# Performance work log

Measured on AMD Instinct MI355X. Metric: run time of the kernel, lower is better.

Reference implementation:

```python
import jax, jax.numpy as jnp
import numpy as np
import math

B, N, C = 2, 1024, 81            # images, proposals per image, classes (incl. background)
IMG_W, IMG_H = 1333, 800         # image size for all images (box.size)
SCORE_THRESH = 0.05
NMS_THRESH = 0.5
DETS_PER_IMG = 100
WX, WY, WW, WH = 10.0, 10.0, 5.0, 5.0   # BoxCoder weights
BBOX_XFORM_CLIP = math.log(1000.0 / 16.0)
NEG_INF = -1e30


def setup_inputs() -> dict:
    key = jax.random.key(0)
    k1, k2, k3, k4 = jax.random.split(key, 4)
    class_logits = jax.random.normal(k1, (B * N, C), dtype=jnp.float32)
    box_regression = jax.random.normal(k2, (B * N, C * 4), dtype=jnp.float32)
    # valid xyxy proposal boxes inside the image
    xy = jax.random.uniform(k3, (B * N, 2), dtype=jnp.float32) * jnp.array([IMG_W - 150.0, IMG_H - 150.0], jnp.float32)
    wh = 10.0 + jax.random.uniform(k4, (B * N, 2), dtype=jnp.float32) * 140.0
    proposal_boxes = jnp.concatenate([xy, xy + wh], axis=-1)
    return {"class_logits": class_logits, "box_regression": box_regression, "proposal_boxes": proposal_boxes}


def box_decode(rel_codes, boxes):
    """BoxCoder.decode (maskrcnn-benchmark). rel_codes [M, 4C], boxes [M,4] xyxy -> [M, C, 4]."""
    TO_REMOVE = 1.0
    widths = boxes[:, 2] - boxes[:, 0] + TO_REMOVE
    heights = boxes[:, 3] - boxes[:, 1] + TO_REMOVE
    ctr_x = boxes[:, 0] + 0.5 * widths
    ctr_y = boxes[:, 1] + 0.5 * heights
    dx = rel_codes[:, 0::4] / WX
    dy = rel_codes[:, 1::4] / WY
    dw = jnp.minimum(rel_codes[:, 2::4] / WW, BBOX_XFORM_CLIP)
    dh = jnp.minimum(rel_codes[:, 3::4] / WH, BBOX_XFORM_CLIP)
    pred_ctr_x = dx * widths[:, None] + ctr_x[:, None]
    pred_ctr_y = dy * heights[:, None] + ctr_y[:, None]
    pred_w = jnp.exp(dw) * widths[:, None]
    pred_h = jnp.exp(dh) * heights[:, None]
    x1 = pred_ctr_x - 0.5 * pred_w
    y1 = pred_ctr_y - 0.5 * pred_h
    x2 = pred_ctr_x + 0.5 * pred_w - 1.0
    y2 = pred_ctr_y + 0.5 * pred_h - 1.0
    return jnp.stack([x1, y1, x2, y2], axis=-1)  # [M, C, 4]


def iou_matrix(b):
    """Pairwise IoU with TO_REMOVE=1 convention. b [N,4] -> [N,N]."""
    area = (b[:, 2] - b[:, 0] + 1.0) * (b[:, 3] - b[:, 1] + 1.0)
    lt = jnp.maximum(b[:, None, :2], b[None, :, :2])
    rb = jnp.minimum(b[:, None, 2:], b[None, :, 2:])
    wh = jnp.clip(rb - lt + 1.0, 0.0)
    inter = wh[..., 0] * wh[..., 1]
    return inter / (area[:, None] + area[None, :] - inter)


def nms_keep(boxes, scores, valid):
    """Masked greedy NMS: returns keep mask [N]. Invalid entries never kept/suppress."""
    s = jnp.where(valid, scores, NEG_INF)
    order = jnp.argsort(-s)            # descending score
    b = boxes[order]
    iou = iou_matrix(b)                # [N, N]
    idx = jnp.arange(N)

    def body(i, keep):
        sup = keep[i] & (iou[i] > NMS_THRESH) & (idx > i)
        return keep & ~sup

    keep_sorted = jax.lax.fori_loop(0, N, body, valid[order])
    return jnp.zeros((N,), bool).at[order].set(keep_sorted)


def per_image(prob, boxes):
    """prob [N,C], boxes [N,C,4] -> top-DETS_PER_IMG (boxes, scores, labels)."""
    fg_prob = prob[:, 1:]              # skip background (cls_start_idx=1)
    fg_boxes = boxes[:, 1:]            # [N, C-1, 4]
    valid = fg_prob > SCORE_THRESH
    # per-class masked NMS, vmapped over the class axis
    keep = jax.vmap(nms_keep, in_axes=(1, 1, 1), out_axes=1)(fg_boxes, fg_prob, valid)  # [N, C-1]
    flat_scores = jnp.where(keep, fg_prob, NEG_INF).reshape(-1)       # [(C-1)*N]
    flat_boxes = fg_boxes.reshape(-1, 4)
    flat_labels = jnp.tile(jnp.arange(1, C, dtype=jnp.int64), (N,))   # matches [N, C-1] flatten
    top_s, top_i = jax.lax.top_k(flat_scores, DETS_PER_IMG)
    valid_top = top_s > SCORE_THRESH
    out_scores = jnp.where(valid_top, top_s, 0.0)
    out_boxes = jnp.where(valid_top[:, None], flat_boxes[top_i], 0.0)
    out_labels = jnp.where(valid_top, flat_labels[top_i], -1)
    return out_boxes, out_scores, out_labels


def reference(class_logits, box_regression, proposal_boxes):
    prob = jax.nn.softmax(class_logits, axis=-1)                # [B*N, C]
    decoded = box_decode(box_regression, proposal_boxes)        # [B*N, C, 4]
    # clip_to_image (remove_empty=False), TO_REMOVE=1
    x = jnp.clip(decoded[..., 0::2], 0.0, IMG_W - 1.0)
    y = jnp.clip(decoded[..., 1::2], 0.0, IMG_H - 1.0)
    decoded = jnp.stack([x[..., 0], y[..., 0], x[..., 1], y[..., 1]], axis=-1)
    prob = prob.reshape(B, N, C)
    decoded = decoded.reshape(B, N, C, 4)
    # process images sequentially to bound the [C-1, N, N] IoU working set
    boxes_out, scores_out, labels_out = jax.lax.map(lambda a: per_image(*a), (prob, decoded))
    return boxes_out, scores_out, labels_out
```

## Files before the change

kernel.cpp:

```cpp
#include <hip/hip_runtime.h>
#include <math.h>

#define B_ 2
#define N_ 1024
#define C_ 81
#define NFG 80
#define DETS 100
#define CAND (N_ * NFG)
#define SCORE_THRESH 0.05f
#define NMS_THRESH 0.5f
#define NEG_INF -1e30f
#define IMG_W_M1 1332.0f
#define IMG_H_M1 799.0f
#define XFORM_CLIP 4.135166556742356f
#define HB 192
#define LCAP 512
#define NROW (B_ * N_)


__device__ __forceinline__ void decode_box(const float* __restrict__ breg,
                                           const float* __restrict__ pbox,
                                           int row, int c, float* out) {
    float bx1 = pbox[row * 4 + 0];
    float by1 = pbox[row * 4 + 1];
    float bx2 = pbox[row * 4 + 2];
    float by2 = pbox[row * 4 + 3];
    float w  = bx2 - bx1 + 1.0f;
    float h  = by2 - by1 + 1.0f;
    float cx = bx1 + 0.5f * w;
    float cy = by1 + 0.5f * h;
    const float* r = breg + (size_t)row * (C_ * 4) + c * 4;
    float dx = r[0] / 10.0f;
    float dy = r[1] / 10.0f;
    float dw = fminf(r[2] / 5.0f, (float)XFORM_CLIP);
    float dh = fminf(r[3] / 5.0f, (float)XFORM_CLIP);
    float px = dx * w + cx;
    float py = dy * h + cy;
    float pw = expf(dw) * w;
    float ph = expf(dh) * h;
    float x1 = px - 0.5f * pw;
    float y1 = py - 0.5f * ph;
    float x2 = px + 0.5f * pw - 1.0f;
    float y2 = py + 0.5f * ph - 1.0f;
    out[0] = fminf(fmaxf(x1, 0.0f), IMG_W_M1);
    out[1] = fminf(fmaxf(y1, 0.0f), IMG_H_M1);
    out[2] = fminf(fmaxf(x2, 0.0f), IMG_W_M1);
    out[3] = fminf(fmaxf(y2, 0.0f), IMG_H_M1);
}


__global__ __launch_bounds__(256) void prob_k(const float* __restrict__ logits,
                                              float* __restrict__ probT,
                                              int* __restrict__ count) {
    if (blockIdx.x == 0 && threadIdx.x < B_) count[threadIdx.x] = 0;
    int row  = blockIdx.x * 4 + (threadIdx.x >> 6);
    int lane = threadIdx.x & 63;
    const float* rp = logits + (size_t)row * C_;
    float v0 = rp[lane];
    float v1 = (lane + 64 < C_) ? rp[lane + 64] : -INFINITY;
    float m = fmaxf(v0, v1);
    #pragma unroll
    for (int off = 32; off; off >>= 1) m = fmaxf(m, __shfl_xor(m, off));
    float e0 = expf(v0 - m);
    float e1 = (lane + 64 < C_) ? expf(v1 - m) : 0.0f;
    float s = e0 + e1;
    #pragma unroll
    for (int off = 32; off; off >>= 1) s += __shfl_xor(s, off);
    probT[(size_t)lane * NROW + row] = e0 / s;
    if (lane + 64 < C_) probT[(size_t)(lane + 64) * NROW + row] = e1 / s;
}


__global__ __launch_bounds__(256) void nms_k(const float* __restrict__ probT,
                                             const float* __restrict__ breg,
                                             const float* __restrict__ pbox,
                                             float* __restrict__ cand_s,
                                             int* __restrict__ cand_i,
                                             int* __restrict__ count) {
    __shared__ float skey[N_];
    __shared__ int   sidx[N_];
    __shared__ float sx1[N_], sy1[N_], sx2[N_], sy2[N_], sar[N_];
    __shared__ unsigned rembits[64];
    __shared__ int   mcount;

    int blk = blockIdx.x;
    int b   = blk / NFG;
    int c   = blk % NFG + 1;
    int tid = threadIdx.x;

    if (tid == 0) mcount = 0;
    __syncthreads();

    const float* col = probT + (size_t)c * NROW + b * N_;
    #pragma unroll
    for (int r = 0; r < N_ / 256; ++r) {
        int n = tid + r * 256;
        float s = col[n];
        if (s > SCORE_THRESH) {
            int p = atomicAdd(&mcount, 1);
            skey[p] = s;
            sidx[p] = n;
        }
    }
    __syncthreads();
    int M = mcount;

    if (M > 0 && M <= 64) {
        if (tid < 64) {
            int lane = tid;
            unsigned long long key;
            if (lane < M)
                key = ((unsigned long long)(~__float_as_uint(skey[lane])) << 32) |
                      (unsigned)sidx[lane];
            else
                key = ~0ULL;
            #pragma unroll
            for (int k = 2; k <= 64; k <<= 1) {
                #pragma unroll
                for (int j = k >> 1; j > 0; j >>= 1) {
                    unsigned long long other = __shfl_xor(key, j);
                    bool lower    = (lane & j) == 0;
                    bool dir_asc  = (lane & k) == 0;
                    bool keep_min = (dir_asc == lower);
                    bool mine_min = key < other;
                    key = (keep_min == mine_min) ? key : other;
                }
            }
            float sc = __uint_as_float(~(unsigned)(key >> 32));
            int   n  = (int)(unsigned)(key & 0xFFFFFFFFu);
            float bx[4]; float area = 0.0f; int rem = 0;
            if (lane < M) {
                decode_box(breg, pbox, b * N_ + n, c, bx);
                area = (bx[2] - bx[0] + 1.0f) * (bx[3] - bx[1] + 1.0f);
            }
            for (int i = 0; i < M; ++i) {
                int   rem_i = __shfl(rem, i);
                float x1i = __shfl(bx[0], i);
                float y1i = __shfl(bx[1], i);
                float x2i = __shfl(bx[2], i);
                float y2i = __shfl(bx[3], i);
                float ai  = __shfl(area, i);
                if (!rem_i && lane > i && lane < M && !rem) {
                    float xx1 = fmaxf(x1i, bx[0]);
                    float yy1 = fmaxf(y1i, bx[1]);
                    float xx2 = fminf(x2i, bx[2]);
                    float yy2 = fminf(y2i, bx[3]);
                    float w = fmaxf(xx2 - xx1 + 1.0f, 0.0f);
                    float h = fmaxf(yy2 - yy1 + 1.0f, 0.0f);
                    float inter = w * h;
                    float iou = inter / (area + ai - inter);
                    if (iou > NMS_THRESH) rem = 1;
                }
            }
            unsigned long long keepmask = __ballot(lane < M && !rem);
            int base = 0;
            if (lane == 0) base = atomicAdd(&count[b], __popcll(keepmask));
            base = __shfl(base, 0);
            if (lane < M && !rem) {
                int pos = base + __popcll(keepmask & ((1ULL << lane) - 1ULL));
                cand_s[(size_t)b * CAND + pos] = sc;
                cand_i[(size_t)b * CAND + pos] = n * NFG + (c - 1);
            }
        }
    } else if (M > 64) {
        int P = 64;
        while (P < M) P <<= 1;
        for (int i = M + tid; i < P; i += 256) { skey[i] = NEG_INF; sidx[i] = 0x7fffffff; }
        __syncthreads();
        for (int k = 2; k <= P; k <<= 1) {
            for (int j = k >> 1; j > 0; j >>= 1) {
                for (int i = tid; i < P; i += 256) {
                    int l = i ^ j;
                    if (l > i) {
                        float ki = skey[i], kl = skey[l];
                        int   ii = sidx[i], il = sidx[l];
                        bool iFirst = (ki > kl) || (ki == kl && ii < il);
                        bool asc = ((i & k) == 0);
                        if (iFirst != asc) {
                            skey[i] = kl; skey[l] = ki;
                            sidx[i] = il; sidx[l] = ii;
                        }
                    }
                }
                __syncthreads();
            }
        }
        for (int i = tid; i < M; i += 256) {
            float box[4];
            decode_box(breg, pbox, b * N_ + sidx[i], c, box);
            sx1[i] = box[0]; sy1[i] = box[1]; sx2[i] = box[2]; sy2[i] = box[3];
            sar[i] = (box[2] - box[0] + 1.0f) * (box[3] - box[1] + 1.0f);
        }
        __syncthreads();
        if (tid < 64) {
            int lane = tid;
            unsigned my = 0;
            for (int i = 0; i < M; ++i) {
                unsigned obits = __shfl(my, i & 63);
                bool kept = ((obits >> (i >> 6)) & 1u) == 0u;
                if (kept) {
                    float x1i = sx1[i], y1i = sy1[i], x2i = sx2[i], y2i = sy2[i], ai = sar[i];
                    for (int j = lane; j < M; j += 64) {
                        if (j > i && !((my >> (j >> 6)) & 1u)) {
                            float xx1 = fmaxf(x1i, sx1[j]);
                            float yy1 = fmaxf(y1i, sy1[j]);
                            float xx2 = fminf(x2i, sx2[j]);
                            float yy2 = fminf(y2i, sy2[j]);
                            float w = fmaxf(xx2 - xx1 + 1.0f, 0.0f);
                            float h = fmaxf(yy2 - yy1 + 1.0f, 0.0f);
                            float inter = w * h;
                            float iou = inter / (ai + sar[j] - inter);
                            if (iou > NMS_THRESH) my |= 1u << (j >> 6);
                        }
                    }
                }
            }
            rembits[lane] = my;
        }
        __syncthreads();
        for (int j = tid; j < M; j += 256) {
            if (!((rembits[j & 63] >> (j >> 6)) & 1u)) {
                int pos = atomicAdd(&count[b], 1);
                cand_s[(size_t)b * CAND + pos] = skey[j];
                cand_i[(size_t)b * CAND + pos] = sidx[j] * NFG + (c - 1);
            }
        }
    }
}


#define TTPB 512

__global__ __launch_bounds__(TTPB) void topk_k(float* __restrict__ cand_s,
                                               const int* __restrict__ cand_i,
                                               const int* __restrict__ count,
                                               const float* __restrict__ breg,
                                               const float* __restrict__ pbox,
                                               float* __restrict__ out) {
    __shared__ int   hist[HB];
    __shared__ int   ssum[HB];
    __shared__ float lsv[LCAP];
    __shared__ int   lfv[LCAP];
    __shared__ int   lcnt;
    __shared__ int   sel_t1;
    __shared__ float rs[TTPB];
    __shared__ int   rf[TTPB];
    __shared__ int   rp[TTPB];

    int b   = blockIdx.x;
    int tid = threadIdx.x;
    int M2  = count[b];
    float* cs = cand_s + (size_t)b * CAND;
    const int* ci = cand_i + (size_t)b * CAND;
    float* boxes_o  = out + (size_t)b * DETS * 4;
    float* scores_o = out + (size_t)B_ * DETS * 4 + (size_t)b * DETS;
    float* labels_o = out + (size_t)B_ * DETS * 4 + (size_t)B_ * DETS + (size_t)b * DETS;

    for (int i = tid; i < HB; i += TTPB) hist[i] = 0;
    if (tid == 0) { lcnt = 0; sel_t1 = 0; }
    __syncthreads();

    for (int i = tid; i < M2; i += TTPB) {
        unsigned bits = __float_as_uint(cs[i]);
        int cb = (int)((bits - 0x3D000000u) >> 18);
        if (cb > HB - 1) cb = HB - 1;
        atomicAdd(&hist[cb], 1);
    }
    __syncthreads();

    if (tid < HB) {
        int acc = 0;
        for (int j = tid; j < HB; ++j) acc += hist[j];
        ssum[tid] = acc;
    }
    __syncthreads();
    if (M2 > DETS && tid < HB) {
        if (ssum[tid] >= DETS && (tid == HB - 1 || ssum[tid + 1] < DETS)) sel_t1 = tid;
    }
    __syncthreads();
    int t1 = sel_t1;

    for (int i = tid; i < M2; i += TTPB) {
        float s = cs[i];
        unsigned bits = __float_as_uint(s);
        int cb = (int)((bits - 0x3D000000u) >> 18);
        if (cb > HB - 1) cb = HB - 1;
        if (cb >= t1) {
            int p = atomicAdd(&lcnt, 1);
            if (p < LCAP) { lsv[p] = s; lfv[p] = ci[i]; }
        }
    }
    __syncthreads();
    int L = lcnt;

    if (L <= LCAP) {
        for (int e = tid; e < L; e += TTPB) {
            float s = lsv[e]; int f = lfv[e];
            int r = 0;
            for (int q = 0; q < L; ++q) {
                float sq = lsv[q]; int fq = lfv[q];
                if (sq > s || (sq == s && fq < f)) r++;
            }
            if (r < DETS) {
                int n = f / NFG;
                int cc = f % NFG + 1;
                float box[4];
                decode_box(breg, pbox, b * N_ + n, cc, box);
                boxes_o[r * 4 + 0] = box[0];
                boxes_o[r * 4 + 1] = box[1];
                boxes_o[r * 4 + 2] = box[2];
                boxes_o[r * 4 + 3] = box[3];
                scores_o[r] = s;
                labels_o[r] = (float)cc;
            }
        }
        int start = (L < DETS) ? L : DETS;
        for (int r = tid; r < DETS; r += TTPB) {
            if (r >= start) {
                boxes_o[r * 4 + 0] = 0.0f;
                boxes_o[r * 4 + 1] = 0.0f;
                boxes_o[r * 4 + 2] = 0.0f;
                boxes_o[r * 4 + 3] = 0.0f;
                scores_o[r] = 0.0f;
                labels_o[r] = -1.0f;
            }
        }
    } else {
        for (int it = 0; it < DETS; ++it) {
            float bs = NEG_INF; int bf = 0x7fffffff; int bp = -1;
            for (int i = tid; i < M2; i += TTPB) {
                float s = cs[i]; int f = ci[i];
                if (s > bs || (s == bs && f < bf)) { bs = s; bf = f; bp = i; }
            }
            rs[tid] = bs; rf[tid] = bf; rp[tid] = bp;
            __syncthreads();
            for (int off = TTPB / 2; off; off >>= 1) {
                if (tid < off) {
                    if (rs[tid + off] > rs[tid] ||
                        (rs[tid + off] == rs[tid] && rf[tid + off] < rf[tid])) {
                        rs[tid] = rs[tid + off]; rf[tid] = rf[tid + off]; rp[tid] = rp[tid + off];
                    }
                }
                __syncthreads();
            }
            if (tid == 0) {
                float s = rs[0];
                bool valid = s > SCORE_THRESH;
                float box[4] = {0.f, 0.f, 0.f, 0.f};
                float lab = -1.0f, scv = 0.0f;
                if (valid) {
                    int fi = rf[0];
                    int n = fi / NFG;
                    int cc = fi % NFG + 1;
                    decode_box(breg, pbox, b * N_ + n, cc, box);
                    lab = (float)cc; scv = s;
                    cs[rp[0]] = NEG_INF;
                }
                boxes_o[it * 4 + 0] = box[0];
                boxes_o[it * 4 + 1] = box[1];
                boxes_o[it * 4 + 2] = box[2];
                boxes_o[it * 4 + 3] = box[3];
                scores_o[it] = scv;
                labels_o[it] = lab;
            }
            __syncthreads();
        }
    }
}


extern "C" void kernel_launch(void* const* d_in, const int* in_sizes, int n_in,
                              void* d_out, int out_size, void* d_ws, size_t ws_size,
                              hipStream_t stream) {
    const float* logits = (const float*)d_in[0];
    const float* breg   = (const float*)d_in[1];
    const float* pbox   = (const float*)d_in[2];
    float* out = (float*)d_out;

    float* cand_s = (float*)d_ws;
    int*   cand_i = (int*)(cand_s + (size_t)B_ * CAND);
    int*   count  = (int*)(cand_i + (size_t)B_ * CAND);
    float* probT  = (float*)(count + 2);

    prob_k<<<NROW / 4, 256, 0, stream>>>(logits, probT, count);
    nms_k<<<B_ * NFG, 256, 0, stream>>>(probT, breg, pbox, cand_s, cand_i, count);
    topk_k<<<B_, TTPB, 0, stream>>>(cand_s, cand_i, count, breg, pbox, out);
}
```

Measured before the change: 38.47 us.

## Replace small-M bitonic sort and serial NMS with rank sort and IoU bitmask

```diff
diff --git a/kernel.cpp b/kernel.cpp
--- a/kernel.cpp
+++ b/kernel.cpp
@@ -82,6 +82,8 @@
     __shared__ float sx1[N_], sy1[N_], sx2[N_], sy2[N_], sar[N_];
     __shared__ unsigned rembits[64];
     __shared__ int   mcount;
+    __shared__ float fs[64];  __shared__ int ffi[64];
+    __shared__ float fx1[64], fy1[64], fx2[64], fy2[64], far_[64];
 
     int blk = blockIdx.x;
     int b   = blk / NFG;
@@ -108,58 +110,60 @@
     if (M > 0 && M <= 64) {
         if (tid < 64) {
             int lane = tid;
-            unsigned long long key;
-            if (lane < M)
-                key = ((unsigned long long)(~__float_as_uint(skey[lane])) << 32) |
-                      (unsigned)sidx[lane];
-            else
-                key = ~0ULL;
-            #pragma unroll
-            for (int k = 2; k <= 64; k <<= 1) {
-                #pragma unroll
-                for (int j = k >> 1; j > 0; j >>= 1) {
-                    unsigned long long other = __shfl_xor(key, j);
-                    bool lower    = (lane & j) == 0;
-                    bool dir_asc  = (lane & k) == 0;
-                    bool keep_min = (dir_asc == lower);
-                    bool mine_min = key < other;
-                    key = (keep_min == mine_min) ? key : other;
-                }
-            }
-            float sc = __uint_as_float(~(unsigned)(key >> 32));
-            int   n  = (int)(unsigned)(key & 0xFFFFFFFFu);
-            float bx[4]; float area = 0.0f; int rem = 0;
             if (lane < M) {
-                decode_box(breg, pbox, b * N_ + n, c, bx);
-                area = (bx[2] - bx[0] + 1.0f) * (bx[3] - bx[1] + 1.0f);
-            }
+                float s = skey[lane];
+                int idx = sidx[lane];
+                int r = 0;
+                for (int q = 0; q < M; ++q) {
+                    float sq = skey[q]; int iq = sidx[q];
+                    if (sq > s || (sq == s && iq < idx)) r++;
+                }
+                float bx[4];
+                decode_box(breg, pbox, b * N_ + idx, c, bx);
+                fs[r]  = s;
+                ffi[r] = idx;
+                fx1[r] = bx[0]; fy1[r] = bx[1]; fx2[r] = bx[2]; fy2[r] = bx[3];
+                far_[r] = (bx[2] - bx[0] + 1.0f) * (bx[3] - bx[1] + 1.0f);
+            }
+        }
+        __syncthreads();
+        if (tid < 64) {
+            int lane = tid;
+            bool act = lane < M;
+            float s = 0.0f, x1 = 0.f, y1 = 0.f, x2 = 0.f, y2 = 0.f, ar = 0.f;
+            int idx = 0;
+            if (act) {
+                s = fs[lane]; idx = ffi[lane];
+                x1 = fx1[lane]; y1 = fy1[lane]; x2 = fx2[lane]; y2 = fy2[lane];
+                ar = far_[lane];
+            }
+            unsigned long long adj = 0ULL;
             for (int i = 0; i < M; ++i) {
-                int   rem_i = __shfl(rem, i);
-                float x1i = __shfl(bx[0], i);
-                float y1i = __shfl(bx[1], i);
-                float x2i = __shfl(bx[2], i);
-                float y2i = __shfl(bx[3], i);
-                float ai  = __shfl(area, i);
-                if (!rem_i && lane > i && lane < M && !rem) {
-                    float xx1 = fmaxf(x1i, bx[0]);
-                    float yy1 = fmaxf(y1i, bx[1]);
-                    float xx2 = fminf(x2i, bx[2]);
-                    float yy2 = fminf(y2i, bx[3]);
+                if (act && i < lane) {
+                    float xx1 = fmaxf(x1, fx1[i]);
+                    float yy1 = fmaxf(y1, fy1[i]);
+                    float xx2 = fminf(x2, fx2[i]);
+                    float yy2 = fminf(y2, fy2[i]);
                     float w = fmaxf(xx2 - xx1 + 1.0f, 0.0f);
                     float h = fmaxf(yy2 - yy1 + 1.0f, 0.0f);
                     float inter = w * h;
-                    float iou = inter / (area + ai - inter);
-                    if (iou > NMS_THRESH) rem = 1;
-                }
-            }
-            unsigned long long keepmask = __ballot(lane < M && !rem);
+                    float iou = inter / (ar + far_[i] - inter);
+                    if (iou > NMS_THRESH) adj |= 1ULL << i;
+                }
+            }
+            int rem = 0;
+            for (int i = 0; i < M; ++i) {
+                unsigned long long remmask = __ballot(rem != 0);
+                if (!((remmask >> i) & 1ULL) && ((adj >> i) & 1ULL)) rem = 1;
+            }
+            unsigned long long keepmask = __ballot(act && !rem);
             int base = 0;
             if (lane == 0) base = atomicAdd(&count[b], __popcll(keepmask));
             base = __shfl(base, 0);
-            if (lane < M && !rem) {
+            if (act && !rem) {
                 int pos = base + __popcll(keepmask & ((1ULL << lane) - 1ULL));
-                cand_s[(size_t)b * CAND + pos] = sc;
-                cand_i[(size_t)b * CAND + pos] = n * NFG + (c - 1);
+                cand_s[(size_t)b * CAND + pos] = s;
+                cand_i[(size_t)b * CAND + pos] = idx * NFG + (c - 1);
             }
         }
     } else if (M > 64) {
```

After: 40.30 us. +4.7%, slower.
